# Performance work log

Hardware: AMD Instinct MI355X
Metric: run time of the kernel (lower is better)

Reference implementation:

```python
import jax, jax.numpy as jnp
import numpy as np

C_IN = 256
C_INT = 128  # in_channels // reduction
SHAPE = (2, C_IN, 8, 32, 32)  # B,C,T,H,W


def setup_inputs() -> dict:
    key = jax.random.key(0)
    ks = jax.random.split(key, 9)
    s = 1.0 / np.sqrt(C_IN)
    si = 1.0 / np.sqrt(C_INT)
    return {
        "x": jax.random.normal(ks[0], SHAPE, dtype=jnp.float32),
        "g_w": jax.random.uniform(ks[1], (C_INT, C_IN), jnp.float32, -s, s),
        "g_b": jax.random.uniform(ks[2], (C_INT,), jnp.float32, -s, s),
        "theta_w": jax.random.uniform(ks[3], (C_INT, C_IN), jnp.float32, -s, s),
        "theta_b": jax.random.uniform(ks[4], (C_INT,), jnp.float32, -s, s),
        "phi_w": jax.random.uniform(ks[5], (C_INT, C_IN), jnp.float32, -s, s),
        "phi_b": jax.random.uniform(ks[6], (C_INT,), jnp.float32, -s, s),
        "w_w": jax.random.uniform(ks[7], (C_IN, C_INT), jnp.float32, -si, si),
        "w_b": jax.random.uniform(ks[8], (C_IN,), jnp.float32, -si, si),
    }


def reference(x, g_w, g_b, theta_w, theta_b, phi_w, phi_b, w_w, w_b):
    B, C, T, H, W = x.shape
    N = T * H * W
    xf = x.reshape(B, C, N)  # 1x1x1 conv == channel matmul on flattened tokens
    g_x = jnp.einsum('bcn,oc->bno', xf, g_w) + g_b            # [B,N,d]
    theta_x = jnp.einsum('bcn,oc->bno', xf, theta_w) + theta_b  # [B,N,d]
    phi_x = jnp.einsum('bcn,oc->bon', xf, phi_w) + phi_b[None, :, None]  # [B,d,N]
    f = jnp.einsum('bnd,bdm->bnm', theta_x, phi_x)            # [B,N,N] (no scaling, as in source)
    f_div_C = jax.nn.softmax(f, axis=-1)
    y = jnp.einsum('bnm,bmd->bnd', f_div_C, g_x)              # [B,N,d]
    y = y.transpose(0, 2, 1).reshape(B, C_INT, T, H, W)
    W_y = jnp.einsum('bdthw,cd->bcthw', y, w_w) + w_b[None, :, None, None, None]
    return W_y + x
```

## Files before the change

kernel.cpp:

```cpp
#include <hip/hip_runtime.h>
#include <hip/hip_bf16.h>
#include <math.h>

#define B_ 2
#define CIN 256
#define D_ 128
#define N_ 8192
#define SPLITS 2
#define KVB 64

typedef unsigned short u16;
typedef unsigned long long u64;
typedef __attribute__((ext_vector_type(8))) short short8;
typedef __attribute__((ext_vector_type(4))) short short4v;
typedef __attribute__((ext_vector_type(4))) float f32x4;

#define NEG_BIG (-1.0e30f)

__device__ __forceinline__ u16 f2bf(float f) {
  union { float f; unsigned u; } v; v.f = f;
  unsigned r = v.u + 0x7fffu + ((v.u >> 16) & 1u);
  return (u16)(r >> 16);
}
__device__ __forceinline__ float bf2f(u16 h) {
  union { unsigned u; float f; } v; v.u = ((unsigned)h) << 16;
  return v.f;
}
__device__ __forceinline__ float expclamp(float x) {
  return __expf(fmaxf(x, -80.0f));
}
__device__ __forceinline__ f32x4 mfma16(short8 a, short8 b, f32x4 c) {
  return __builtin_amdgcn_mfma_f32_16x16x32_bf16(a, b, c, 0, 0, 0);
}
__device__ __forceinline__ u64 pack4(float a, float b, float c, float d) {
  return (u64)f2bf(a) | ((u64)f2bf(b) << 16) | ((u64)f2bf(c) << 32) |
         ((u64)f2bf(d) << 48);
}

__global__ __launch_bounds__(256) void wcvt_kernel(
    const float* __restrict__ th_w, const float* __restrict__ ph_w,
    const float* __restrict__ g_w, const float* __restrict__ w_w,
    u16* __restrict__ Wt, u16* __restrict__ Wp, u16* __restrict__ Wg,
    u16* __restrict__ Wm) {
  const int s = blockIdx.y;
  const float* src = s == 0 ? th_w : (s == 1 ? ph_w : (s == 2 ? g_w : w_w));
  u16* dst = s == 0 ? Wt : (s == 1 ? Wp : (s == 2 ? Wg : Wm));
  const int i = (blockIdx.x * 256 + threadIdx.x) * 4;
  const float4 v = *reinterpret_cast<const float4*>(&src[i]);
  *reinterpret_cast<u64*>(&dst[i]) = pack4(v.x, v.y, v.z, v.w);
}

__global__ __launch_bounds__(512) void proj_mfma(
    const float* __restrict__ x, const u16* __restrict__ Wt,
    const u16* __restrict__ Wp, const u16* __restrict__ Wg,
    const float* __restrict__ th_b, const float* __restrict__ ph_b,
    const float* __restrict__ g_b, u16* __restrict__ Qg,
    u16* __restrict__ Kg, u16* __restrict__ Vtg) {
  __shared__ __align__(16) u16 xT[64][256];
  const int t = threadIdx.x;
  const int b = blockIdx.y, n0 = blockIdx.x * 64;
  {
    const int n = t & 63, ph = t >> 6;
#pragma unroll
    for (int it = 0; it < 8; ++it) {
      const int c0 = it * 32 + ph * 4;
      const size_t base = ((size_t)b * CIN + c0) * N_ + n0 + n;
      const float v0 = x[base];
      const float v1 = x[base + N_];
      const float v2 = x[base + 2 * N_];
      const float v3 = x[base + 3 * N_];
      const int cs = c0 ^ ((n & 7) << 3);
      *reinterpret_cast<u64*>(&xT[n][cs]) = pack4(v0, v1, v2, v3);
    }
  }
  __syncthreads();

  const int lane = t & 63, wv = t >> 6;
  const int l15 = lane & 15, hi = lane >> 4;
  const int tg = wv & 3, oh = wv >> 2;
  const int nrow = tg * 16 + l15;

  short8 xa[8];
#pragma unroll
  for (int ks = 0; ks < 8; ++ks) {
    const int c = (ks * 32 + hi * 8) ^ ((nrow & 7) << 3);
    xa[ks] = *reinterpret_cast<const short8*>(&xT[nrow][c]);
  }

  const size_t qrow = ((size_t)b * N_ + n0 + tg * 16 + l15) * D_;
#pragma unroll
  for (int pp = 0; pp < 2; ++pp) {
    const u16* W = pp ? Wp : Wt;
    const float* bias = pp ? ph_b : th_b;
    u16* out = pp ? Kg : Qg;
#pragma unroll
    for (int os = 0; os < 4; ++os) {
      const int ob = oh * 64 + os * 16;
      short8 wf[8];
#pragma unroll
      for (int ks = 0; ks < 8; ++ks)
        wf[ks] = *reinterpret_cast<const short8*>(
            &W[(size_t)(ob + l15) * CIN + ks * 32 + hi * 8]);
      f32x4 acc = {0.f, 0.f, 0.f, 0.f};
#pragma unroll
      for (int ks = 0; ks < 8; ++ks) acc = mfma16(wf[ks], xa[ks], acc);
      const float4 bb = *reinterpret_cast<const float4*>(&bias[ob + hi * 4]);
      *reinterpret_cast<u64*>(&out[qrow + ob + hi * 4]) =
          pack4(acc[0] + bb.x, acc[1] + bb.y, acc[2] + bb.z, acc[3] + bb.w);
    }
  }
#pragma unroll
  for (int os = 0; os < 4; ++os) {
    const int ob = oh * 64 + os * 16;
    short8 wf[8];
#pragma unroll
    for (int ks = 0; ks < 8; ++ks)
      wf[ks] = *reinterpret_cast<const short8*>(
          &Wg[(size_t)(ob + l15) * CIN + ks * 32 + hi * 8]);
    f32x4 acc = {0.f, 0.f, 0.f, 0.f};
#pragma unroll
    for (int ks = 0; ks < 8; ++ks) acc = mfma16(xa[ks], wf[ks], acc);
    const float bs = g_b[ob + l15];
    *reinterpret_cast<u64*>(
        &Vtg[((size_t)b * D_ + ob + l15) * N_ + n0 + tg * 16 + hi * 4]) =
        pack4(acc[0] + bs, acc[1] + bs, acc[2] + bs, acc[3] + bs);
  }
}

__global__ __launch_bounds__(256) void attn_kernel(
    const u16* __restrict__ Qg, const u16* __restrict__ Kg,
    const u16* __restrict__ Vtg, u16* __restrict__ Opart,
    float2* __restrict__ stats) {
  __shared__ __align__(16) u16 Ks[2][KVB][136];
  __shared__ __align__(16) u16 Vs[2][D_][72];
  const int t = threadIdx.x;
  const int wv = t >> 6, lane = t & 63;
  const int l15 = lane & 15, hi = lane >> 4;
  const int qb = blockIdx.x, b = blockIdx.y, sp = blockIdx.z;
  const int q0 = qb * 128 + wv * 32;
  const size_t key0 = (size_t)sp * (N_ / SPLITS);
  const int NT = (N_ / SPLITS) / KVB;

  short8 qf[2][4];
#pragma unroll
  for (int qt = 0; qt < 2; ++qt)
#pragma unroll
    for (int ks = 0; ks < 4; ++ks)
      qf[qt][ks] = *reinterpret_cast<const short8*>(
          Qg + ((size_t)b * N_ + q0 + qt * 16 + l15) * D_ + ks * 32 + hi * 8);

  f32x4 oacc[2][8];
#pragma unroll
  for (int qt = 0; qt < 2; ++qt)
#pragma unroll
    for (int ds = 0; ds < 8; ++ds) {
      f32x4 z = {0.f, 0.f, 0.f, 0.f};
      oacc[qt][ds] = z;
    }
  float mrun[2] = {NEG_BIG, NEG_BIG};
  float lrun[2] = {0.f, 0.f};

  const int kr = t >> 4, kseg = t & 15;
  const int vd = t >> 3, vseg = t & 7;

  {
    short8 kv[4], vv[4];
#pragma unroll
    for (int i = 0; i < 4; ++i) {
      kv[i] = *reinterpret_cast<const short8*>(
          Kg + ((size_t)b * N_ + key0 + kr + i * 16) * D_ + kseg * 8);
      vv[i] = *reinterpret_cast<const short8*>(
          Vtg + ((size_t)b * D_ + vd + i * 32) * N_ + key0 + vseg * 8);
    }
#pragma unroll
    for (int i = 0; i < 4; ++i) {
      *reinterpret_cast<short8*>(&Ks[0][kr + i * 16][kseg * 8]) = kv[i];
      *reinterpret_cast<short8*>(&Vs[0][vd + i * 32][vseg * 8]) = vv[i];
    }
  }
  __syncthreads();

  for (int tile = 0; tile < NT; ++tile) {
    const int cur = tile & 1;
    const bool pre = (tile + 1 < NT);
    short8 kv[4], vv[4];
    if (pre) {
      const size_t kb2 = key0 + (size_t)(tile + 1) * KVB;
#pragma unroll
      for (int i = 0; i < 4; ++i) {
        kv[i] = *reinterpret_cast<const short8*>(
            Kg + ((size_t)b * N_ + kb2 + kr + i * 16) * D_ + kseg * 8);
        vv[i] = *reinterpret_cast<const short8*>(
            Vtg + ((size_t)b * D_ + vd + i * 32) * N_ + kb2 + vseg * 8);
      }
    }
    f32x4 sacc[2][4];
#pragma unroll
    for (int qt = 0; qt < 2; ++qt)
#pragma unroll
      for (int sub = 0; sub < 4; ++sub) {
        f32x4 z = {0.f, 0.f, 0.f, 0.f};
        sacc[qt][sub] = z;
      }
#pragma unroll
    for (int sub = 0; sub < 4; ++sub) {
#pragma unroll
      for (int ks = 0; ks < 4; ++ks) {
        const short8 kf = *reinterpret_cast<const short8*>(
            &Ks[cur][sub * 16 + l15][ks * 32 + hi * 8]);
        sacc[0][sub] = mfma16(kf, qf[0][ks], sacc[0][sub]);
        sacc[1][sub] = mfma16(kf, qf[1][ks], sacc[1][sub]);
      }
    }
    short8 paq[2][2];
#pragma unroll
    for (int qt = 0; qt < 2; ++qt) {
      float pmax = NEG_BIG;
#pragma unroll
      for (int sub = 0; sub < 4; ++sub)
#pragma unroll
        for (int r = 0; r < 4; ++r) pmax = fmaxf(pmax, sacc[qt][sub][r]);
      pmax = fmaxf(pmax, __shfl_xor(pmax, 16));
      pmax = fmaxf(pmax, __shfl_xor(pmax, 32));
      const float mnew = fmaxf(mrun[qt], pmax);
      const float scale = expclamp(mrun[qt] - mnew);
      mrun[qt] = mnew;
      float rs = 0.f;
      float p[4][4];
#pragma unroll
      for (int sub = 0; sub < 4; ++sub)
#pragma unroll
        for (int r = 0; r < 4; ++r) {
          p[sub][r] = __expf(sacc[qt][sub][r] - mnew);
          rs += p[sub][r];
        }
      rs += __shfl_xor(rs, 16);
      rs += __shfl_xor(rs, 32);
      lrun[qt] = lrun[qt] * scale + rs;
      float osc[4];
#pragma unroll
      for (int r = 0; r < 4; ++r) osc[r] = __shfl(scale, (hi << 2) + r);
#pragma unroll
      for (int ds = 0; ds < 8; ++ds)
#pragma unroll
        for (int r = 0; r < 4; ++r) oacc[qt][ds][r] *= osc[r];
#pragma unroll
      for (int kb = 0; kb < 2; ++kb)
#pragma unroll
        for (int j = 0; j < 4; ++j) {
          paq[qt][kb][j] = (short)f2bf(p[2 * kb][j]);
          paq[qt][kb][4 + j] = (short)f2bf(p[2 * kb + 1][j]);
        }
    }
#pragma unroll
    for (int ds = 0; ds < 8; ++ds) {
#pragma unroll
      for (int kb = 0; kb < 2; ++kb) {
        const short4v v0 = *reinterpret_cast<const short4v*>(
            &Vs[cur][ds * 16 + l15][kb * 32 + hi * 4]);
        const short4v v1 = *reinterpret_cast<const short4v*>(
            &Vs[cur][ds * 16 + l15][kb * 32 + 16 + hi * 4]);
        short8 vf;
        vf[0] = v0[0]; vf[1] = v0[1]; vf[2] = v0[2]; vf[3] = v0[3];
        vf[4] = v1[0]; vf[5] = v1[1]; vf[6] = v1[2]; vf[7] = v1[3];
        oacc[0][ds] = mfma16(paq[0][kb], vf, oacc[0][ds]);
        oacc[1][ds] = mfma16(paq[1][kb], vf, oacc[1][ds]);
      }
    }
    __syncthreads();
    if (pre) {
      const int nxt = cur ^ 1;
#pragma unroll
      for (int i = 0; i < 4; ++i) {
        *reinterpret_cast<short8*>(&Ks[nxt][kr + i * 16][kseg * 8]) = kv[i];
        *reinterpret_cast<short8*>(&Vs[nxt][vd + i * 32][vseg * 8]) = vv[i];
      }
    }
    __syncthreads();
  }
  const size_t ob = (((size_t)sp * B_ + b) * N_) * D_;
#pragma unroll
  for (int qt = 0; qt < 2; ++qt) {
#pragma unroll
    for (int ds = 0; ds < 8; ++ds)
#pragma unroll
      for (int r = 0; r < 4; ++r) {
        const int q = q0 + qt * 16 + hi * 4 + r;
        Opart[ob + (size_t)q * D_ + ds * 16 + l15] = f2bf(oacc[qt][ds][r]);
      }
    if (hi == 0)
      stats[((size_t)sp * B_ + b) * N_ + q0 + qt * 16 + l15] =
          make_float2(mrun[qt], lrun[qt]);
  }
}

__global__ __launch_bounds__(256) void combine_kernel(
    const u16* __restrict__ Opart, const float2* __restrict__ stats,
    u16* __restrict__ y16) {
  const size_t total = (size_t)B_ * N_ * D_;
  for (size_t i = (size_t)blockIdx.x * 256 + threadIdx.x; i < total;
       i += (size_t)gridDim.x * 256) {
    const size_t bq = i >> 7;
    const float2 s0 = stats[bq];
    const float2 s1 = stats[(size_t)B_ * N_ + bq];
    const float M = fmaxf(s0.x, s1.x);
    const float w0 = expclamp(s0.x - M), w1 = expclamp(s1.x - M);
    const float den = w0 * s0.y + w1 * s1.y;
    const float o0 = bf2f(Opart[i]);
    const float o1 = bf2f(Opart[total + i]);
    y16[i] = f2bf((w0 * o0 + w1 * o1) / den);
  }
}

__global__ __launch_bounds__(512) void final_mfma(
    const u16* __restrict__ y16, const u16* __restrict__ Wm,
    const float* __restrict__ w_b, const float* __restrict__ x,
    float* __restrict__ out) {
  __shared__ __align__(16) u16 yT[64][128];
  const int t = threadIdx.x;
  const int b = blockIdx.y, n0 = blockIdx.x * 64;
  {
    const int dseg = t & 15, nb = t >> 4;
#pragma unroll
    for (int it = 0; it < 2; ++it) {
      const int nn = nb + it * 32;
      const short8 v = *reinterpret_cast<const short8*>(
          &y16[((size_t)b * N_ + n0 + nn) * D_ + dseg * 8]);
      *reinterpret_cast<short8*>(&yT[nn][(dseg * 8) ^ ((nn & 7) << 3)]) = v;
    }
  }
  __syncthreads();
  const int lane = t & 63, wv = t >> 6;
  const int l15 = lane & 15, hi = lane >> 4;
  const int tg = wv & 3, oh = wv >> 2;
  const int nrow = tg * 16 + l15;

  short8 xa[4];
#pragma unroll
  for (int ks = 0; ks < 4; ++ks) {
    const int c = (ks * 32 + hi * 8) ^ ((nrow & 7) << 3);
    xa[ks] = *reinterpret_cast<const short8*>(&yT[nrow][c]);
  }
#pragma unroll
  for (int os = 0; os < 8; ++os) {
    const int ob = oh * 128 + os * 16;
    short8 wf[4];
#pragma unroll
    for (int ks = 0; ks < 4; ++ks)
      wf[ks] = *reinterpret_cast<const short8*>(
          &Wm[(size_t)(ob + l15) * D_ + ks * 32 + hi * 8]);
    f32x4 acc = {0.f, 0.f, 0.f, 0.f};
#pragma unroll
    for (int ks = 0; ks < 4; ++ks) acc = mfma16(xa[ks], wf[ks], acc);
    const int c = ob + l15;
    const float bs = w_b[c];
    const size_t o = ((size_t)b * CIN + c) * N_ + n0 + tg * 16 + hi * 4;
    const float4 xr = *reinterpret_cast<const float4*>(&x[o]);
    float4 r;
    r.x = acc[0] + bs + xr.x;
    r.y = acc[1] + bs + xr.y;
    r.z = acc[2] + bs + xr.z;
    r.w = acc[3] + bs + xr.w;
    *reinterpret_cast<float4*>(&out[o]) = r;
  }
}

extern "C" void kernel_launch(void* const* d_in, const int* in_sizes, int n_in,
                              void* d_out, int out_size, void* d_ws,
                              size_t ws_size, hipStream_t stream) {
  const float* x = (const float*)d_in[0];
  const float* g_w = (const float*)d_in[1];
  const float* g_b = (const float*)d_in[2];
  const float* th_w = (const float*)d_in[3];
  const float* th_b = (const float*)d_in[4];
  const float* ph_w = (const float*)d_in[5];
  const float* ph_b = (const float*)d_in[6];
  const float* w_w = (const float*)d_in[7];
  const float* w_b = (const float*)d_in[8];
  float* out = (float*)d_out;

  char* ws = (char*)d_ws;
  u16* y16 = (u16*)ws;
  u16* Qg = (u16*)ws;    ws += (size_t)B_ * N_ * D_ * 2;
  u16* Kg = (u16*)ws;    ws += (size_t)B_ * N_ * D_ * 2;
  u16* Vtg = (u16*)ws;   ws += (size_t)B_ * N_ * D_ * 2;
  u16* Opart = (u16*)ws; ws += (size_t)SPLITS * B_ * N_ * D_ * 2;
  float2* stats = (float2*)ws; ws += (size_t)SPLITS * B_ * N_ * sizeof(float2);
  u16* Wt = (u16*)ws;    ws += (size_t)128 * 256 * 2;
  u16* Wp = (u16*)ws;    ws += (size_t)128 * 256 * 2;
  u16* Wg = (u16*)ws;    ws += (size_t)128 * 256 * 2;
  u16* Wm = (u16*)ws;    ws += (size_t)256 * 128 * 2;

  wcvt_kernel<<<dim3(32, 4), 256, 0, stream>>>(th_w, ph_w, g_w, w_w,
                                               Wt, Wp, Wg, Wm);
  proj_mfma<<<dim3(N_ / 64, B_), 512, 0, stream>>>(
      x, Wt, Wp, Wg, th_b, ph_b, g_b, Qg, Kg, Vtg);
  attn_kernel<<<dim3(N_ / 128, B_, SPLITS), 256, 0, stream>>>(
      Qg, Kg, Vtg, Opart, stats);
  combine_kernel<<<dim3(2048), 256, 0, stream>>>(Opart, stats, y16);
  final_mfma<<<dim3(N_ / 64, B_), 512, 0, stream>>>(y16, Wm, w_b, x, out);
}
```

Before: 276.2 us.

## Split attention work across 8 waves with 16 queries each instead of 4 waves

The attention kernel now launches 512 threads per block, with each wave owning one 16-query tile instead of two, so per-thread accumulator and Q-fragment registers are halved. The K/V tile loads into shared memory are redistributed across the larger thread count. This is meant to raise occupancy and latency hiding. The cost is that each K/V fragment read from LDS now feeds only one MFMA instead of two, which doubles LDS traffic per unit of compute, and block-wide syncs now involve more waves.

```diff
diff --git a/kernel.cpp b/kernel.cpp
--- a/kernel.cpp
+++ b/kernel.cpp
@@ -127,7 +127,7 @@
   }
 }
 
-__global__ __launch_bounds__(256) void attn_kernel(
+__global__ __launch_bounds__(512) void attn_kernel(
     const u16* __restrict__ Qg, const u16* __restrict__ Kg,
     const u16* __restrict__ Vtg, u16* __restrict__ Opart,
     float2* __restrict__ stats) {
@@ -137,45 +137,39 @@
   const int wv = t >> 6, lane = t & 63;
   const int l15 = lane & 15, hi = lane >> 4;
   const int qb = blockIdx.x, b = blockIdx.y, sp = blockIdx.z;
-  const int q0 = qb * 128 + wv * 32;
+  const int q0 = qb * 128 + wv * 16;
   const size_t key0 = (size_t)sp * (N_ / SPLITS);
   const int NT = (N_ / SPLITS) / KVB;
 
-  short8 qf[2][4];
-#pragma unroll
-  for (int qt = 0; qt < 2; ++qt)
-#pragma unroll
-    for (int ks = 0; ks < 4; ++ks)
-      qf[qt][ks] = *reinterpret_cast<const short8*>(
-          Qg + ((size_t)b * N_ + q0 + qt * 16 + l15) * D_ + ks * 32 + hi * 8);
-
-  f32x4 oacc[2][8];
-#pragma unroll
-  for (int qt = 0; qt < 2; ++qt)
-#pragma unroll
-    for (int ds = 0; ds < 8; ++ds) {
-      f32x4 z = {0.f, 0.f, 0.f, 0.f};
-      oacc[qt][ds] = z;
-    }
-  float mrun[2] = {NEG_BIG, NEG_BIG};
-  float lrun[2] = {0.f, 0.f};
-
-  const int kr = t >> 4, kseg = t & 15;
-  const int vd = t >> 3, vseg = t & 7;
+  short8 qf[4];
+#pragma unroll
+  for (int ks = 0; ks < 4; ++ks)
+    qf[ks] = *reinterpret_cast<const short8*>(
+        Qg + ((size_t)b * N_ + q0 + l15) * D_ + ks * 32 + hi * 8);
+
+  f32x4 oacc[8];
+#pragma unroll
+  for (int ds = 0; ds < 8; ++ds) {
+    f32x4 z = {0.f, 0.f, 0.f, 0.f};
+    oacc[ds] = z;
+  }
+  float mrun = NEG_BIG, lrun = 0.f;
 
   {
-    short8 kv[4], vv[4];
-#pragma unroll
-    for (int i = 0; i < 4; ++i) {
-      kv[i] = *reinterpret_cast<const short8*>(
-          Kg + ((size_t)b * N_ + key0 + kr + i * 16) * D_ + kseg * 8);
-      vv[i] = *reinterpret_cast<const short8*>(
-          Vtg + ((size_t)b * D_ + vd + i * 32) * N_ + key0 + vseg * 8);
-    }
-#pragma unroll
-    for (int i = 0; i < 4; ++i) {
-      *reinterpret_cast<short8*>(&Ks[0][kr + i * 16][kseg * 8]) = kv[i];
-      *reinterpret_cast<short8*>(&Vs[0][vd + i * 32][vseg * 8]) = vv[i];
+    short8 kv[2], vv[2];
+#pragma unroll
+    for (int it = 0; it < 2; ++it) {
+      const int ks_ = it * 512 + t, vs_ = it * 512 + t;
+      kv[it] = *reinterpret_cast<const short8*>(
+          Kg + ((size_t)b * N_ + key0 + (ks_ >> 4)) * D_ + (ks_ & 15) * 8);
+      vv[it] = *reinterpret_cast<const short8*>(
+          Vtg + ((size_t)b * D_ + (vs_ >> 3)) * N_ + key0 + (vs_ & 7) * 8);
+    }
+#pragma unroll
+    for (int it = 0; it < 2; ++it) {
+      const int ks_ = it * 512 + t, vs_ = it * 512 + t;
+      *reinterpret_cast<short8*>(&Ks[0][ks_ >> 4][(ks_ & 15) * 8]) = kv[it];
+      *reinterpret_cast<short8*>(&Vs[0][vs_ >> 3][(vs_ & 7) * 8]) = vv[it];
     }
   }
   __syncthreads();
@@ -183,75 +177,70 @@
   for (int tile = 0; tile < NT; ++tile) {
     const int cur = tile & 1;
     const bool pre = (tile + 1 < NT);
-    short8 kv[4], vv[4];
+    short8 kv[2], vv[2];
     if (pre) {
       const size_t kb2 = key0 + (size_t)(tile + 1) * KVB;
 #pragma unroll
-      for (int i = 0; i < 4; ++i) {
-        kv[i] = *reinterpret_cast<const short8*>(
-            Kg + ((size_t)b * N_ + kb2 + kr + i * 16) * D_ + kseg * 8);
-        vv[i] = *reinterpret_cast<const short8*>(
-            Vtg + ((size_t)b * D_ + vd + i * 32) * N_ + kb2 + vseg * 8);
-      }
-    }
-    f32x4 sacc[2][4];
-#pragma unroll
-    for (int qt = 0; qt < 2; ++qt)
-#pragma unroll
-      for (int sub = 0; sub < 4; ++sub) {
-        f32x4 z = {0.f, 0.f, 0.f, 0.f};
-        sacc[qt][sub] = z;
-      }
+      for (int it = 0; it < 2; ++it) {
+        const int ks_ = it * 512 + t, vs_ = it * 512 + t;
+        kv[it] = *reinterpret_cast<const short8*>(
+            Kg + ((size_t)b * N_ + kb2 + (ks_ >> 4)) * D_ + (ks_ & 15) * 8);
+        vv[it] = *reinterpret_cast<const short8*>(
+            Vtg + ((size_t)b * D_ + (vs_ >> 3)) * N_ + kb2 + (vs_ & 7) * 8);
+      }
+    }
+    f32x4 sacc[4];
+#pragma unroll
+    for (int sub = 0; sub < 4; ++sub) {
+      f32x4 z = {0.f, 0.f, 0.f, 0.f};
+      sacc[sub] = z;
+    }
 #pragma unroll
     for (int sub = 0; sub < 4; ++sub) {
 #pragma unroll
       for (int ks = 0; ks < 4; ++ks) {
         const short8 kf = *reinterpret_cast<const short8*>(
             &Ks[cur][sub * 16 + l15][ks * 32 + hi * 8]);
-        sacc[0][sub] = mfma16(kf, qf[0][ks], sacc[0][sub]);
-        sacc[1][sub] = mfma16(kf, qf[1][ks], sacc[1][sub]);
-      }
-    }
-    short8 paq[2][2];
-#pragma unroll
-    for (int qt = 0; qt < 2; ++qt) {
-      float pmax = NEG_BIG;
-#pragma unroll
-      for (int sub = 0; sub < 4; ++sub)
-#pragma unroll
-        for (int r = 0; r < 4; ++r) pmax = fmaxf(pmax, sacc[qt][sub][r]);
-      pmax = fmaxf(pmax, __shfl_xor(pmax, 16));
-      pmax = fmaxf(pmax, __shfl_xor(pmax, 32));
-      const float mnew = fmaxf(mrun[qt], pmax);
-      const float scale = expclamp(mrun[qt] - mnew);
-      mrun[qt] = mnew;
-      float rs = 0.f;
-      float p[4][4];
-#pragma unroll
-      for (int sub = 0; sub < 4; ++sub)
-#pragma unroll
-        for (int r = 0; r < 4; ++r) {
-          p[sub][r] = __expf(sacc[qt][sub][r] - mnew);
-          rs += p[sub][r];
-        }
-      rs += __shfl_xor(rs, 16);
-      rs += __shfl_xor(rs, 32);
-      lrun[qt] = lrun[qt] * scale + rs;
-      float osc[4];
-#pragma unroll
-      for (int r = 0; r < 4; ++r) osc[r] = __shfl(scale, (hi << 2) + r);
-#pragma unroll
-      for (int ds = 0; ds < 8; ++ds)
-#pragma unroll
-        for (int r = 0; r < 4; ++r) oacc[qt][ds][r] *= osc[r];
-#pragma unroll
-      for (int kb = 0; kb < 2; ++kb)
-#pragma unroll
-        for (int j = 0; j < 4; ++j) {
-          paq[qt][kb][j] = (short)f2bf(p[2 * kb][j]);
-          paq[qt][kb][4 + j] = (short)f2bf(p[2 * kb + 1][j]);
-        }
-    }
+        sacc[sub] = mfma16(kf, qf[ks], sacc[sub]);
+      }
+    }
+    float pmax = NEG_BIG;
+#pragma unroll
+    for (int sub = 0; sub < 4; ++sub)
+#pragma unroll
+      for (int r = 0; r < 4; ++r) pmax = fmaxf(pmax, sacc[sub][r]);
+    pmax = fmaxf(pmax, __shfl_xor(pmax, 16));
+    pmax = fmaxf(pmax, __shfl_xor(pmax, 32));
+    const float mnew = fmaxf(mrun, pmax);
+    const float scale = expclamp(mrun - mnew);
+    mrun = mnew;
+    float rs = 0.f;
+    float p[4][4];
+#pragma unroll
+    for (int sub = 0; sub < 4; ++sub)
+#pragma unroll
+      for (int r = 0; r < 4; ++r) {
+        p[sub][r] = __expf(sacc[sub][r] - mnew);
+        rs += p[sub][r];
+      }
+    rs += __shfl_xor(rs, 16);
+    rs += __shfl_xor(rs, 32);
+    lrun = lrun * scale + rs;
+    float osc[4];
+#pragma unroll
+    for (int r = 0; r < 4; ++r) osc[r] = __shfl(scale, (hi << 2) + r);
+#pragma unroll
+    for (int ds = 0; ds < 8; ++ds)
+#pragma unroll
+      for (int r = 0; r < 4; ++r) oacc[ds][r] *= osc[r];
+    short8 paq[2];
+#pragma unroll
+    for (int kb = 0; kb < 2; ++kb)
+#pragma unroll
+      for (int j = 0; j < 4; ++j) {
+        paq[kb][j] = (short)f2bf(p[2 * kb][j]);
+        paq[kb][4 + j] = (short)f2bf(p[2 * kb + 1][j]);
+      }
 #pragma unroll
     for (int ds = 0; ds < 8; ++ds) {
 #pragma unroll
@@ -263,35 +252,31 @@
         short8 vf;
         vf[0] = v0[0]; vf[1] = v0[1]; vf[2] = v0[2]; vf[3] = v0[3];
         vf[4] = v1[0]; vf[5] = v1[1]; vf[6] = v1[2]; vf[7] = v1[3];
-        oacc[0][ds] = mfma16(paq[0][kb], vf, oacc[0][ds]);
-        oacc[1][ds] = mfma16(paq[1][kb], vf, oacc[1][ds]);
+        oacc[ds] = mfma16(paq[kb], vf, oacc[ds]);
       }
     }
     __syncthreads();
     if (pre) {
       const int nxt = cur ^ 1;
 #pragma unroll
-      for (int i = 0; i < 4; ++i) {
-        *reinterpret_cast<short8*>(&Ks[nxt][kr + i * 16][kseg * 8]) = kv[i];
-        *reinterpret_cast<short8*>(&Vs[nxt][vd + i * 32][vseg * 8]) = vv[i];
+      for (int it = 0; it < 2; ++it) {
+        const int ks_ = it * 512 + t, vs_ = it * 512 + t;
+        *reinterpret_cast<short8*>(&Ks[nxt][ks_ >> 4][(ks_ & 15) * 8]) = kv[it];
+        *reinterpret_cast<short8*>(&Vs[nxt][vs_ >> 3][(vs_ & 7) * 8]) = vv[it];
       }
     }
     __syncthreads();
   }
   const size_t ob = (((size_t)sp * B_ + b) * N_) * D_;
 #pragma unroll
-  for (int qt = 0; qt < 2; ++qt) {
-#pragma unroll
-    for (int ds = 0; ds < 8; ++ds)
-#pragma unroll
-      for (int r = 0; r < 4; ++r) {
-        const int q = q0 + qt * 16 + hi * 4 + r;
-        Opart[ob + (size_t)q * D_ + ds * 16 + l15] = f2bf(oacc[qt][ds][r]);
-      }
-    if (hi == 0)
-      stats[((size_t)sp * B_ + b) * N_ + q0 + qt * 16 + l15] =
-          make_float2(mrun[qt], lrun[qt]);
-  }
+  for (int ds = 0; ds < 8; ++ds)
+#pragma unroll
+    for (int r = 0; r < 4; ++r) {
+      const int q = q0 + hi * 4 + r;
+      Opart[ob + (size_t)q * D_ + ds * 16 + l15] = f2bf(oacc[ds][r]);
+    }
+  if (hi == 0)
+    stats[((size_t)sp * B_ + b) * N_ + q0 + l15] = make_float2(mrun, lrun);
 }
 
 __global__ __launch_bounds__(256) void combine_kernel(
@@ -395,7 +380,7 @@
                                                Wt, Wp, Wg, Wm);
   proj_mfma<<<dim3(N_ / 64, B_), 512, 0, stream>>>(
       x, Wt, Wp, Wg, th_b, ph_b, g_b, Qg, Kg, Vtg);
-  attn_kernel<<<dim3(N_ / 128, B_, SPLITS), 256, 0, stream>>>(
+  attn_kernel<<<dim3(N_ / 128, B_, SPLITS), 512, 0, stream>>>(
       Qg, Kg, Vtg, Opart, stats);
   combine_kernel<<<dim3(2048), 256, 0, stream>>>(Opart, stats, y16);
   final_mfma<<<dim3(N_ / 64, B_), 512, 0, stream>>>(y16, Wm, w_b, x, out);
```

Result: faster. 262.1 us (-5.1%).
